# Performance work log

Measured on AMD Instinct MI355X. Metric: run time of the kernel, lower is better.

Reference implementation:

```python
import jax, jax.numpy as jnp
import numpy as np

B, N, D, H = 4, 4096, 1024, 16
DH = D // H            # 64
GH = 4 * DH            # gate hidden = 256
FREQ = N // 2 + 1      # 2049
INV_SQRT2 = 0.7071067811865476


def _ln(x, g, b, eps=1e-6):
    mu = jnp.mean(x, axis=-1, keepdims=True)
    var = jnp.mean((x - mu) ** 2, axis=-1, keepdims=True)
    return (x - mu) / jnp.sqrt(var + eps) * g + b


def _xavier(k, out_f, in_f, gain=0.8):
    bound = gain * (6.0 / (in_f + out_f)) ** 0.5
    return jax.random.uniform(k, (out_f, in_f), jnp.float32, -bound, bound)


def setup_inputs() -> dict:
    key = jax.random.key(0)
    ks = jax.random.split(key, 8)
    return {
        'x': jax.random.normal(ks[0], (B, N, D), jnp.float32),
        'Wq': _xavier(ks[1], D, D),
        'Wv': _xavier(ks[2], D, D),
        'Wo': _xavier(ks[3], D, D),
        'ln_g': jnp.ones((DH,), jnp.float32),
        'ln_b': jnp.zeros((DH,), jnp.float32),
        'Wgup': _xavier(ks[4], GH, DH),
        'Wgdn': _xavier(ks[5], 2 * FREQ, GH),
        'Wwup': _xavier(ks[6], GH, DH),
        'Wwdn': _xavier(ks[7], N, GH),
    }


def reference(x, Wq, Wv, Wo, ln_g, ln_b, Wgup, Wgdn, Wwup, Wwdn):
    Bx, Nx, Dx = x.shape
    # projections -> [B, H, N, DH]
    q = (x @ Wq.T).reshape(Bx, Nx, H, DH).transpose(0, 2, 1, 3)
    v = (x @ Wv.T).reshape(Bx, Nx, H, DH).transpose(0, 2, 1, 3)
    # per-head summary token -> complex spectral gate over FREQ bins
    bar = _ln(q.mean(axis=2), ln_g, ln_b)                    # [B, H, DH]
    gr = (jax.nn.silu(bar @ Wgup.T) @ Wgdn.T)               # [B, H, 2*FREQ]
    gr = gr.reshape(Bx, H, FREQ, 2)
    gate = jax.lax.complex(gr[..., 0], gr[..., 1])           # [B, H, FREQ]
    # spectral mixing (chunk == seq_len, power-of-two path)
    spec = jnp.fft.rfft(v, axis=2, norm='ortho') * gate[..., None]
    v_t = jnp.fft.irfft(spec, n=Nx, axis=2, norm='ortho')    # [B, H, N, DH]
    # Haar wavelet refinement
    even, odd = v_t[..., ::2, :], v_t[..., 1::2, :]
    w = jnp.concatenate([even + odd, even - odd], axis=-2) * INV_SQRT2
    s = (jax.nn.silu(bar @ Wwup.T) @ Wwdn.T)[..., None]      # [B, H, N, 1]
    w = w * s
    half = Nx // 2
    low, high = w[..., :half, :], w[..., half:, :]
    # interleave even/odd back along seq dim
    refine = jnp.stack([low + high, low - high], axis=-2).reshape(Bx, H, Nx, DH) * INV_SQRT2
    v_t = v_t + refine
    y = v_t.transpose(0, 2, 1, 3).reshape(Bx, Nx, Dx)
    return y @ Wo.T
```

## Files before the change

### kernel.cpp

```cpp
#include <hip/hip_runtime.h>

constexpr int CB = 4, CN = 4096, CD = 1024, CH = 16, CDH = 64, CGH = 256, CFREQ = 2049, CBH = 64;

constexpr size_t OFF_XSUM = 0;
constexpr size_t OFF_HG   = 4096;
constexpr size_t OFF_HW   = OFF_HG + (size_t)CBH * CGH;
constexpr size_t OFF_GATE = OFF_HW + (size_t)CBH * CGH;
constexpr size_t OFF_S    = OFF_GATE + (size_t)CBH * 2 * CFREQ;
constexpr size_t OFF_CA   = OFF_S + (size_t)CBH * CN;
constexpr size_t OFF_CD   = OFF_CA + (size_t)CBH * (CN / 2);
constexpr size_t OFF_TW   = OFF_CD + (size_t)CBH * (CN / 2);
constexpr size_t OFF_VCOL = OFF_TW + 8192;
constexpr size_t OFF_XHI  = OFF_VCOL + (size_t)CB * CD * CN;
constexpr size_t OFF_XLO  = OFF_XHI + (size_t)CB * CN * CD / 2;
constexpr size_t OFF_WVHI = OFF_XLO + (size_t)CB * CN * CD / 2;
constexpr size_t OFF_WVLO = OFF_WVHI + (size_t)CD * CD / 2;
constexpr size_t OFF_WOHI = OFF_WVLO + (size_t)CD * CD / 2;
constexpr size_t OFF_WOLO = OFF_WOHI + (size_t)CD * CD / 2;

typedef __bf16 bf16x8 __attribute__((ext_vector_type(8)));
typedef __bf16 bf16x4 __attribute__((ext_vector_type(4)));
typedef float  f32x4  __attribute__((ext_vector_type(4)));

__device__ __forceinline__ float silu_f(float x) { return x / (1.0f + expf(-x)); }

__device__ __forceinline__ void gload16(const void* g, void* l) {
    __builtin_amdgcn_global_load_lds(
        reinterpret_cast<const __attribute__((address_space(1))) unsigned int*>(
            reinterpret_cast<uintptr_t>(g)),
        reinterpret_cast<__attribute__((address_space(3))) unsigned int*>(
            reinterpret_cast<uintptr_t>(l)),
        16, 0, 0);
}

__device__ __forceinline__ float2 cadd(float2 a, float2 b) { return make_float2(a.x + b.x, a.y + b.y); }
__device__ __forceinline__ float2 csub(float2 a, float2 b) { return make_float2(a.x - b.x, a.y - b.y); }
__device__ __forceinline__ float2 cmul(float2 a, float2 b) { return make_float2(a.x * b.x - a.y * b.y, a.x * b.y + a.y * b.x); }
__device__ __forceinline__ float2 cmulc(float2 a, float2 b) { return make_float2(a.x * b.x + a.y * b.y, a.y * b.x - a.x * b.y); }
__device__ __forceinline__ float2 mulni(float2 a) { return make_float2(a.y, -a.x); }
__device__ __forceinline__ float2 mulpi(float2 a) { return make_float2(-a.y, a.x); }

__device__ __forceinline__ int fsw(int r) { return r ^ ((r >> 4) & 15); }

__device__ __forceinline__ int drev4(int k) {
    return ((k & 3) << 10) | (((k >> 2) & 3) << 8) | (((k >> 4) & 3) << 6)
         | (((k >> 6) & 3) << 4) | (((k >> 8) & 3) << 2) | ((k >> 10) & 3);
}

__global__ void k_tw(float* twf) {
    int i = blockIdx.x * 256 + threadIdx.x;
    if (i < 4096) {
        double ang = -2.0 * 3.14159265358979323846 * (double)i / 4096.0;
        twf[2 * i]     = (float)cos(ang);
        twf[2 * i + 1] = (float)sin(ang);
    }
}

__global__ __launch_bounds__(256) void k_meansplit(const float* __restrict__ X, float* __restrict__ xsum,
                                                   __bf16* __restrict__ hi, __bf16* __restrict__ lo) {
    int b = blockIdx.y;
    int c = blockIdx.x;
    int t = threadIdx.x;
    int half = t >> 7;
    int col = (t & 127) * 8;
    size_t base = (size_t)b * CN * CD + ((size_t)c * 64 + half * 32) * CD + col;
    float acc[8];
#pragma unroll
    for (int j = 0; j < 8; ++j) acc[j] = 0.f;
    for (int n = 0; n < 32; ++n) {
        size_t o = base + (size_t)n * CD;
        float4 v0 = *(const float4*)(X + o);
        float4 v1 = *(const float4*)(X + o + 4);
        float vv[8] = {v0.x, v0.y, v0.z, v0.w, v1.x, v1.y, v1.z, v1.w};
        bf16x8 hv, lv;
#pragma unroll
        for (int j = 0; j < 8; ++j) {
            acc[j] += vv[j];
            __bf16 h = (__bf16)vv[j];
            hv[j] = h;
            lv[j] = (__bf16)(vv[j] - (float)h);
        }
        *(bf16x8*)&hi[o] = hv;
        *(bf16x8*)&lo[o] = lv;
    }
#pragma unroll
    for (int j = 0; j < 8; ++j) atomicAdd(&xsum[b * CD + col + j], acc[j]);
}

__global__ __launch_bounds__(256) void k_barhidden(const float* __restrict__ xsum,
                                                   const float* __restrict__ Wq,
                                                   const float* __restrict__ ln_g,
                                                   const float* __restrict__ ln_b,
                                                   const float* __restrict__ Wgup,
                                                   const float* __restrict__ Wwup,
                                                   float* __restrict__ hg, float* __restrict__ hw) {
    int bh = blockIdx.x;
    int b = bh >> 4, h = bh & 15;
    int t = threadIdx.x;
    __shared__ float part[256];
    __shared__ float bar_s[64];
    int dh = t >> 2, seg = t & 3;
    const float* wrow = Wq + (size_t)(h * 64 + dh) * CD + seg * 256;
    const float* xs = xsum + b * CD + seg * 256;
    float acc = 0.f;
    for (int i = 0; i < 256; i += 4) {
        float4 w4 = *(const float4*)(wrow + i);
        float4 x4 = *(const float4*)(xs + i);
        acc += w4.x * x4.x + w4.y * x4.y + w4.z * x4.z + w4.w * x4.w;
    }
    part[t] = acc;
    __syncthreads();
    if (t < 64) {
        float q = (part[4 * t] + part[4 * t + 1] + part[4 * t + 2] + part[4 * t + 3]) * (1.0f / 4096.0f);
        float mu = q;
        for (int o = 32; o >= 1; o >>= 1) mu += __shfl_xor(mu, o, 64);
        mu *= (1.0f / 64.0f);
        float dev = q - mu;
        float vv = dev * dev;
        for (int o = 32; o >= 1; o >>= 1) vv += __shfl_xor(vv, o, 64);
        vv *= (1.0f / 64.0f);
        bar_s[t] = dev / sqrtf(vv + 1e-6f) * ln_g[t] + ln_b[t];
    }
    __syncthreads();
    const float* gup = Wgup + (size_t)t * CDH;
    const float* wup = Wwup + (size_t)t * CDH;
    float ag = 0.f, aw = 0.f;
    for (int i = 0; i < CDH; i += 4) {
        float4 bb = *(const float4*)(&bar_s[i]);
        float4 g4 = *(const float4*)(gup + i);
        float4 w4 = *(const float4*)(wup + i);
        ag += g4.x * bb.x + g4.y * bb.y + g4.z * bb.z + g4.w * bb.w;
        aw += w4.x * bb.x + w4.y * bb.y + w4.z * bb.z + w4.w * bb.w;
    }
    hg[bh * CGH + t] = silu_f(ag);
    hw[bh * CGH + t] = silu_f(aw);
}

__global__ __launch_bounds__(256) void k_gategemv(const float* __restrict__ Wgdn,
                                                  const float* __restrict__ Wwdn,
                                                  const float* __restrict__ hg,
                                                  const float* __restrict__ hw,
                                                  float* __restrict__ gate, float* __restrict__ sbuf) {
    int z = blockIdx.z;
    const float* Wd = z ? Wwdn : Wgdn;
    const float* hid = z ? hw : hg;
    float* out = z ? sbuf : gate;
    int Kout = z ? CN : 2 * CFREQ;
    int bh0 = blockIdx.y * 8;
    int t = threadIdx.x;
    int k = blockIdx.x * 256 + t;
    __shared__ float Lh[8][256];
    for (int g = 0; g < 8; ++g) Lh[g][t] = hid[(size_t)(bh0 + g) * CGH + t];
    __syncthreads();
    if (k >= Kout) return;
    float accv[8] = {0.f, 0.f, 0.f, 0.f, 0.f, 0.f, 0.f, 0.f};
    const float* wrow = Wd + (size_t)k * CGH;
    for (int j4 = 0; j4 < 64; ++j4) {
        float4 wv = *(const float4*)(wrow + 4 * j4);
#pragma unroll
        for (int g = 0; g < 8; ++g) {
            accv[g] += wv.x * Lh[g][4 * j4] + wv.y * Lh[g][4 * j4 + 1] +
                       wv.z * Lh[g][4 * j4 + 2] + wv.w * Lh[g][4 * j4 + 3];
        }
    }
    for (int g = 0; g < 8; ++g) out[(size_t)(bh0 + g) * Kout + k] = accv[g];
}

__global__ __launch_bounds__(256) void k_coef(const float* __restrict__ sbuf,
                                              float* __restrict__ ca, float* __restrict__ cd) {
    int bh = blockIdx.y;
    int i = blockIdx.x * 256 + threadIdx.x;
    float s0 = sbuf[(size_t)bh * CN + i];
    float s1 = sbuf[(size_t)bh * CN + 2048 + i];
    ca[(size_t)bh * 2048 + i] = 1.0f + 0.5f * (s0 + s1);
    cd[(size_t)bh * 2048 + i] = 0.5f * (s0 - s1);
}

__global__ __launch_bounds__(256) void k_split(const float* __restrict__ src,
                                               __bf16* __restrict__ hi, __bf16* __restrict__ lo,
                                               int n4) {
    int i = blockIdx.x * 256 + threadIdx.x;
    int stride = gridDim.x * 256;
    for (; i < n4; i += stride) {
        float4 v = ((const float4*)src)[i];
        __bf16 h0 = (__bf16)v.x, h1 = (__bf16)v.y, h2 = (__bf16)v.z, h3 = (__bf16)v.w;
        bf16x4 hv = {h0, h1, h2, h3};
        bf16x4 lv = {(__bf16)(v.x - (float)h0), (__bf16)(v.y - (float)h1),
                     (__bf16)(v.z - (float)h2), (__bf16)(v.w - (float)h3)};
        *(bf16x4*)&hi[4 * (size_t)i] = hv;
        *(bf16x4*)&lo[4 * (size_t)i] = lv;
    }
}

__global__ __launch_bounds__(256) void k_tsplit(const float* __restrict__ Vcol,
                                                __bf16* __restrict__ hi, __bf16* __restrict__ lo) {
    __shared__ float tile[32][33];
    int bx = blockIdx.x;
    int by = blockIdx.y;
    int b  = blockIdx.z;
    int t = threadIdx.x;
    int d = t >> 3, n4 = (t & 7) * 4;
    const float* src = Vcol + ((size_t)b * CD + by * 32 + d) * CN + bx * 32 + n4;
    float4 v = *(const float4*)src;
    tile[d][n4] = v.x; tile[d][n4 + 1] = v.y; tile[d][n4 + 2] = v.z; tile[d][n4 + 3] = v.w;
    __syncthreads();
    int n = t >> 3, d4 = (t & 7) * 4;
    size_t o = ((size_t)b * CN + bx * 32 + n) * CD + by * 32 + d4;
    float x0 = tile[d4][n], x1 = tile[d4 + 1][n], x2 = tile[d4 + 2][n], x3 = tile[d4 + 3][n];
    __bf16 h0 = (__bf16)x0, h1 = (__bf16)x1, h2 = (__bf16)x2, h3 = (__bf16)x3;
    bf16x4 hv = {h0, h1, h2, h3};
    bf16x4 lv = {(__bf16)(x0 - (float)h0), (__bf16)(x1 - (float)h1),
                 (__bf16)(x2 - (float)h2), (__bf16)(x3 - (float)h3)};
    *(bf16x4*)&hi[o] = hv;
    *(bf16x4*)&lo[o] = lv;
}

template <int TRANS>
__global__ __launch_bounds__(256) void k_mfma_gemm(const __bf16* __restrict__ Ahi,
                                                   const __bf16* __restrict__ Alo,
                                                   const __bf16* __restrict__ Bhi,
                                                   const __bf16* __restrict__ Blo,
                                                   float* __restrict__ C) {
    __shared__ __align__(16) __bf16 lds[2][4][128 * 32];
    int t = threadIdx.x;
    int l = t & 63, w = t >> 6;
    int hw = blockIdx.x + (blockIdx.y << 3);
    int xcd = hw & 7, slot = hw >> 3;
    int m0 = (xcd * 16 + (slot >> 3)) * 128;
    int n0 = (slot & 7) * 128;
    int wm = w >> 1, wn = w & 1;

    const __bf16* gsrc = (w == 0) ? Ahi : (w == 1) ? Alo : (w == 2) ? Bhi : Blo;
    int gr0 = (w < 2) ? m0 : n0;
    unsigned o[8];
#pragma unroll
    for (int i = 0; i < 8; ++i) {
        int row = i * 16 + (l >> 2);
        unsigned slotq = (unsigned)((l & 3) ^ ((row >> 2) & 3));
        o[i] = (unsigned)(gr0 + row) * 1024u + slotq * 8u;
    }

    f32x4 acc[4][4];
#pragma unroll
    for (int m = 0; m < 4; ++m)
#pragma unroll
        for (int n = 0; n < 4; ++n) acc[m][n] = (f32x4){0.f, 0.f, 0.f, 0.f};

#pragma unroll
    for (int i = 0; i < 8; ++i)
        gload16(gsrc + (size_t)o[i], &lds[0][w][i * 512]);
    __syncthreads();

    int cur = 0;
#pragma unroll 2
    for (int k0 = 0; k0 < 1024; k0 += 32) {
        if (k0 + 32 < 1024) {
#pragma unroll
            for (int i = 0; i < 8; ++i)
                gload16(gsrc + ((size_t)o[i] + k0 + 32), &lds[cur ^ 1][w][i * 512]);
        }

        bf16x8 ah[4], al[4], bh[4], bl[4];
#pragma unroll
        for (int m = 0; m < 4; ++m) {
            int row = wm * 64 + m * 16 + (l & 15);
            int sl = (l >> 4) ^ ((row >> 2) & 3);
            ah[m] = *(const bf16x8*)&lds[cur][0][row * 32 + sl * 8];
            al[m] = *(const bf16x8*)&lds[cur][1][row * 32 + sl * 8];
        }
#pragma unroll
        for (int n = 0; n < 4; ++n) {
            int row = wn * 64 + n * 16 + (l & 15);
            int sl = (l >> 4) ^ ((row >> 2) & 3);
            bh[n] = *(const bf16x8*)&lds[cur][2][row * 32 + sl * 8];
            bl[n] = *(const bf16x8*)&lds[cur][3][row * 32 + sl * 8];
        }
#pragma unroll
        for (int m = 0; m < 4; ++m)
#pragma unroll
            for (int n = 0; n < 4; ++n) {
                acc[m][n] = __builtin_amdgcn_mfma_f32_16x16x32_bf16(ah[m], bh[n], acc[m][n], 0, 0, 0);
                acc[m][n] = __builtin_amdgcn_mfma_f32_16x16x32_bf16(ah[m], bl[n], acc[m][n], 0, 0, 0);
                acc[m][n] = __builtin_amdgcn_mfma_f32_16x16x32_bf16(al[m], bh[n], acc[m][n], 0, 0, 0);
            }
        __syncthreads();
        cur ^= 1;
    }

    if (TRANS) {
        int b = m0 >> 12;
        int tokb = (m0 & 4095) + wm * 64;
#pragma unroll
        for (int m = 0; m < 4; ++m)
#pragma unroll
            for (int n = 0; n < 4; ++n) {
                int dcol = n0 + wn * 64 + n * 16 + (l & 15);
                int tok = tokb + m * 16 + ((l >> 4) << 2);
                *(f32x4*)&C[((size_t)(b * CD + dcol)) * CN + tok] = acc[m][n];
            }
    } else {
#pragma unroll
        for (int m = 0; m < 4; ++m)
#pragma unroll
            for (int n = 0; n < 4; ++n) {
                int r0 = m0 + wm * 64 + m * 16 + ((l >> 4) << 2);
                int cc = n0 + wn * 64 + n * 16 + (l & 15);
#pragma unroll
                for (int q = 0; q < 4; ++q) C[(size_t)(r0 + q) * CD + cc] = acc[m][n][q];
            }
    }
}

__global__ __launch_bounds__(512) void k_fft(float* __restrict__ Vcol,
                                             const float* __restrict__ gateB,
                                             const float* __restrict__ caB,
                                             const float* __restrict__ cdB,
                                             const float2* __restrict__ tw) {
    __shared__ float2 buf[4096];
    int blk = blockIdx.x;
    int bh = blk >> 5, pr = blk & 31;
    int t = threadIdx.x;
    float* colA = Vcol + (size_t)(bh * 64 + pr * 2) * CN;
    float* colB = colA + CN;

    for (int n = t; n < 4096; n += 512) buf[fsw(n)] = make_float2(colA[n], colB[n]);
    __syncthreads();

#pragma unroll 1
    for (int M = 1024; M >= 1; M >>= 2) {
        int tstep = 1024 / M;
        for (int idx = t; idx < 1024; idx += 512) {
            int j = idx & (M - 1);
            int i0 = ((idx & ~(M - 1)) << 2) + j;
            float2 a0 = buf[fsw(i0)];
            float2 a1 = buf[fsw(i0 + M)];
            float2 a2 = buf[fsw(i0 + 2 * M)];
            float2 a3 = buf[fsw(i0 + 3 * M)];
            float2 t0 = cadd(a0, a2), t1 = csub(a0, a2);
            float2 t2 = cadd(a1, a3), t3 = csub(a1, a3);
            float2 w1 = tw[j * tstep], w2 = tw[2 * j * tstep], w3 = tw[3 * j * tstep];
            buf[fsw(i0)]         = cadd(t0, t2);
            buf[fsw(i0 + M)]     = cmul(cadd(t1, mulni(t3)), w1);
            buf[fsw(i0 + 2 * M)] = cmul(csub(t0, t2), w2);
            buf[fsw(i0 + 3 * M)] = cmul(cadd(t1, mulpi(t3)), w3);
        }
        __syncthreads();
    }

    const float2* g2 = (const float2*)gateB + (size_t)bh * CFREQ;
    for (int k = t; k <= 2048; k += 512) {
        int r  = drev4(k);
        int r2 = drev4((4096 - k) & 4095);
        float2 Zk = buf[fsw(r)];
        float2 Zj = buf[fsw(r2)];
        float2 Av = make_float2(0.5f * (Zk.x + Zj.x), 0.5f * (Zk.y - Zj.y));
        float2 Bv = make_float2(0.5f * (Zk.y + Zj.y), -0.5f * (Zk.x - Zj.x));
        float2 g = g2[k];
        float2 SA = cmul(g, Av);
        float2 SB = cmul(g, Bv);
        buf[fsw(r)] = make_float2(SA.x - SB.y, SA.y + SB.x);
        if (r2 != r) buf[fsw(r2)] = make_float2(SA.x + SB.y, SB.x - SA.y);
    }
    __syncthreads();

#pragma unroll 1
    for (int M = 1; M <= 1024; M <<= 2) {
        int tstep = 1024 / M;
        for (int idx = t; idx < 1024; idx += 512) {
            int j = idx & (M - 1);
            int i0 = ((idx & ~(M - 1)) << 2) + j;
            float2 a0 = buf[fsw(i0)];
            float2 a1 = cmulc(buf[fsw(i0 + M)], tw[j * tstep]);
            float2 a2 = cmulc(buf[fsw(i0 + 2 * M)], tw[2 * j * tstep]);
            float2 a3 = cmulc(buf[fsw(i0 + 3 * M)], tw[3 * j * tstep]);
            float2 t0 = cadd(a0, a2), t1 = csub(a0, a2);
            float2 t2 = cadd(a1, a3), t3 = csub(a1, a3);
            buf[fsw(i0)]         = cadd(t0, t2);
            buf[fsw(i0 + M)]     = cadd(t1, mulpi(t3));
            buf[fsw(i0 + 2 * M)] = csub(t0, t2);
            buf[fsw(i0 + 3 * M)] = csub(t1, mulpi(t3));
        }
        __syncthreads();
    }

    const float scale = 1.0f / 4096.0f;
    const float* ca = caB + (size_t)bh * 2048;
    const float* cd = cdB + (size_t)bh * 2048;
    for (int i = t; i < 2048; i += 512) {
        float2 v0 = buf[fsw(2 * i)], v1 = buf[fsw(2 * i + 1)];
        float a0x = v0.x * scale, a1x = v1.x * scale;
        float a0y = v0.y * scale, a1y = v1.y * scale;
        float A_ = ca[i], D_ = cd[i];
        *(float2*)(colA + 2 * i) = make_float2(A_ * a0x + D_ * a1x, D_ * a0x + A_ * a1x);
        *(float2*)(colB + 2 * i) = make_float2(A_ * a0y + D_ * a1y, D_ * a0y + A_ * a1y);
    }
}

extern "C" void kernel_launch(void* const* d_in, const int* in_sizes, int n_in,
                              void* d_out, int out_size, void* d_ws, size_t ws_size,
                              hipStream_t stream) {
    const float* x    = (const float*)d_in[0];
    const float* Wq   = (const float*)d_in[1];
    const float* Wv   = (const float*)d_in[2];
    const float* Wo   = (const float*)d_in[3];
    const float* ln_g = (const float*)d_in[4];
    const float* ln_b = (const float*)d_in[5];
    const float* Wgup = (const float*)d_in[6];
    const float* Wgdn = (const float*)d_in[7];
    const float* Wwup = (const float*)d_in[8];
    const float* Wwdn = (const float*)d_in[9];
    float* ws  = (float*)d_ws;
    float* out = (float*)d_out;

    __bf16* xhi  = (__bf16*)(ws + OFF_XHI);
    __bf16* xlo  = (__bf16*)(ws + OFF_XLO);
    __bf16* wvhi = (__bf16*)(ws + OFF_WVHI);
    __bf16* wvlo = (__bf16*)(ws + OFF_WVLO);
    __bf16* wohi = (__bf16*)(ws + OFF_WOHI);
    __bf16* wolo = (__bf16*)(ws + OFF_WOLO);
    __bf16* v2hi = (__bf16*)(ws + OFF_XHI);
    __bf16* v2lo = (__bf16*)(ws + OFF_XLO);

    hipMemsetAsync(ws + OFF_XSUM, 0, 4096 * sizeof(float), stream);
    k_tw<<<16, 256, 0, stream>>>(ws + OFF_TW);
    k_meansplit<<<dim3(64, 4), 256, 0, stream>>>(x, ws + OFF_XSUM, xhi, xlo);
    k_barhidden<<<64, 256, 0, stream>>>(ws + OFF_XSUM, Wq, ln_g, ln_b, Wgup, Wwup,
                                        ws + OFF_HG, ws + OFF_HW);
    k_gategemv<<<dim3(17, 8, 2), 256, 0, stream>>>(Wgdn, Wwdn, ws + OFF_HG, ws + OFF_HW,
                                                   ws + OFF_GATE, ws + OFF_S);
    k_coef<<<dim3(8, 64), 256, 0, stream>>>(ws + OFF_S, ws + OFF_CA, ws + OFF_CD);

    k_split<<<1024, 256, 0, stream>>>(Wv, wvhi, wvlo, CD * CD / 4);
    k_split<<<1024, 256, 0, stream>>>(Wo, wohi, wolo, CD * CD / 4);

    k_mfma_gemm<1><<<dim3(8, 128), 256, 0, stream>>>(xhi, xlo, wvhi, wvlo, ws + OFF_VCOL);

    k_fft<<<2048, 512, 0, stream>>>(ws + OFF_VCOL, ws + OFF_GATE, ws + OFF_CA, ws + OFF_CD,
                                    (const float2*)(ws + OFF_TW));

    k_tsplit<<<dim3(128, 32, 4), 256, 0, stream>>>(ws + OFF_VCOL, v2hi, v2lo);

    k_mfma_gemm<0><<<dim3(8, 128), 256, 0, stream>>>(v2hi, v2lo, wohi, wolo, out);
}
```

Measured before the change: 425.6 us.

## Switch spectral FFT from radix-4 to radix-8 with fused first and last stages

Replaces the six-stage radix-4 shared-memory FFT with a four-stage radix-8 decomposition. The first forward stage runs straight from global loads and the last inverse stage feeds the Haar refinement output through lane shuffles, so fewer LDS round trips and barriers are needed. LDS indexing changes from an XOR swizzle to a padded layout, and the scale factor is folded into the wavelet coefficients. This raises register pressure per thread and depends on the twiddle table indexing and the radix-8 digit-reversal being correct.

```diff
diff --git a/kernel.cpp b/kernel.cpp
--- a/kernel.cpp
+++ b/kernel.cpp
@@ -40,11 +40,78 @@
 __device__ __forceinline__ float2 mulni(float2 a) { return make_float2(a.y, -a.x); }
 __device__ __forceinline__ float2 mulpi(float2 a) { return make_float2(-a.y, a.x); }
 
-__device__ __forceinline__ int fsw(int r) { return r ^ ((r >> 4) & 15); }
-
-__device__ __forceinline__ int drev4(int k) {
-    return ((k & 3) << 10) | (((k >> 2) & 3) << 8) | (((k >> 4) & 3) << 6)
-         | (((k >> 6) & 3) << 4) | (((k >> 8) & 3) << 2) | ((k >> 10) & 3);
+__device__ __forceinline__ int P(int r) { return r + (r >> 3); }
+
+__device__ __forceinline__ int drev8(int k) {
+    return ((k & 7) << 9) | (((k >> 3) & 7) << 6) | (((k >> 6) & 7) << 3) | ((k >> 9) & 7);
+}
+
+__device__ __forceinline__ void dft8_fwd(const float2 a[8], float2 A[8]) {
+    float2 t0 = cadd(a[0], a[4]), t1 = csub(a[0], a[4]);
+    float2 t2 = cadd(a[2], a[6]), t3 = mulni(csub(a[2], a[6]));
+    float2 t4 = cadd(a[1], a[5]), t5 = csub(a[1], a[5]);
+    float2 t6 = cadd(a[3], a[7]), t7 = mulni(csub(a[3], a[7]));
+    float2 u0 = cadd(t0, t2), u1 = csub(t0, t2);
+    float2 u2 = cadd(t1, t3), u3 = csub(t1, t3);
+    float2 u4 = cadd(t4, t6), u5 = mulni(csub(t4, t6));
+    float2 u6 = cadd(t5, t7), u7 = csub(t5, t7);
+    const float s = 0.70710678118654752f;
+    float2 w6 = make_float2(s * (u6.x + u6.y), s * (u6.y - u6.x));
+    float2 w7 = make_float2(s * (u7.y - u7.x), -s * (u7.x + u7.y));
+    A[0] = cadd(u0, u4); A[4] = csub(u0, u4);
+    A[2] = cadd(u1, u5); A[6] = csub(u1, u5);
+    A[1] = cadd(u2, w6); A[5] = csub(u2, w6);
+    A[3] = cadd(u3, w7); A[7] = csub(u3, w7);
+}
+
+__device__ __forceinline__ void dft8_inv(const float2 a[8], float2 A[8]) {
+    float2 t0 = cadd(a[0], a[4]), t1 = csub(a[0], a[4]);
+    float2 t2 = cadd(a[2], a[6]), t3 = mulpi(csub(a[2], a[6]));
+    float2 t4 = cadd(a[1], a[5]), t5 = csub(a[1], a[5]);
+    float2 t6 = cadd(a[3], a[7]), t7 = mulpi(csub(a[3], a[7]));
+    float2 u0 = cadd(t0, t2), u1 = csub(t0, t2);
+    float2 u2 = cadd(t1, t3), u3 = csub(t1, t3);
+    float2 u4 = cadd(t4, t6), u5 = mulpi(csub(t4, t6));
+    float2 u6 = cadd(t5, t7), u7 = csub(t5, t7);
+    const float s = 0.70710678118654752f;
+    float2 w6 = make_float2(s * (u6.x - u6.y), s * (u6.x + u6.y));
+    float2 w7 = make_float2(-s * (u7.x + u7.y), s * (u7.x - u7.y));
+    A[0] = cadd(u0, u4); A[4] = csub(u0, u4);
+    A[2] = cadd(u1, u5); A[6] = csub(u1, u5);
+    A[1] = cadd(u2, w6); A[5] = csub(u2, w6);
+    A[3] = cadd(u3, w7); A[7] = csub(u3, w7);
+}
+
+template <int M>
+__device__ __forceinline__ void fwd_stage(float2* buf, const float2* __restrict__ tw, int t) {
+    int j = t & (M - 1);
+    int i0 = ((t & ~(M - 1)) << 3) + j;
+    constexpr int TS = 512 / M;
+    float2 a[8], A[8];
+#pragma unroll
+    for (int c = 0; c < 8; ++c) a[c] = buf[P(i0 + c * M)];
+    dft8_fwd(a, A);
+#pragma unroll
+    for (int p = 0; p < 8; ++p) {
+        float2 v = (M > 1 && p) ? cmul(A[p], tw[j * p * TS]) : A[p];
+        buf[P(i0 + p * M)] = v;
+    }
+}
+
+template <int M>
+__device__ __forceinline__ void inv_stage(float2* buf, const float2* __restrict__ tw, int t) {
+    int j = t & (M - 1);
+    int i0 = ((t & ~(M - 1)) << 3) + j;
+    constexpr int TS = 512 / M;
+    float2 a[8], A[8];
+#pragma unroll
+    for (int c = 0; c < 8; ++c) {
+        float2 v = buf[P(i0 + c * M)];
+        a[c] = (M > 1 && c) ? cmulc(v, tw[j * c * TS]) : v;
+    }
+    dft8_inv(a, A);
+#pragma unroll
+    for (int p = 0; p < 8; ++p) buf[P(i0 + p * M)] = A[p];
 }
 
 __global__ void k_tw(float* twf) {
@@ -316,83 +383,75 @@
                                              const float* __restrict__ caB,
                                              const float* __restrict__ cdB,
                                              const float2* __restrict__ tw) {
-    __shared__ float2 buf[4096];
+    __shared__ float2 buf[4608];
     int blk = blockIdx.x;
     int bh = blk >> 5, pr = blk & 31;
     int t = threadIdx.x;
     float* colA = Vcol + (size_t)(bh * 64 + pr * 2) * CN;
     float* colB = colA + CN;
 
-    for (int n = t; n < 4096; n += 512) buf[fsw(n)] = make_float2(colA[n], colB[n]);
-    __syncthreads();
-
-#pragma unroll 1
-    for (int M = 1024; M >= 1; M >>= 2) {
-        int tstep = 1024 / M;
-        for (int idx = t; idx < 1024; idx += 512) {
-            int j = idx & (M - 1);
-            int i0 = ((idx & ~(M - 1)) << 2) + j;
-            float2 a0 = buf[fsw(i0)];
-            float2 a1 = buf[fsw(i0 + M)];
-            float2 a2 = buf[fsw(i0 + 2 * M)];
-            float2 a3 = buf[fsw(i0 + 3 * M)];
-            float2 t0 = cadd(a0, a2), t1 = csub(a0, a2);
-            float2 t2 = cadd(a1, a3), t3 = csub(a1, a3);
-            float2 w1 = tw[j * tstep], w2 = tw[2 * j * tstep], w3 = tw[3 * j * tstep];
-            buf[fsw(i0)]         = cadd(t0, t2);
-            buf[fsw(i0 + M)]     = cmul(cadd(t1, mulni(t3)), w1);
-            buf[fsw(i0 + 2 * M)] = cmul(csub(t0, t2), w2);
-            buf[fsw(i0 + 3 * M)] = cmul(cadd(t1, mulpi(t3)), w3);
-        }
-        __syncthreads();
-    }
-
-    const float2* g2 = (const float2*)gateB + (size_t)bh * CFREQ;
-    for (int k = t; k <= 2048; k += 512) {
-        int r  = drev4(k);
-        int r2 = drev4((4096 - k) & 4095);
-        float2 Zk = buf[fsw(r)];
-        float2 Zj = buf[fsw(r2)];
-        float2 Av = make_float2(0.5f * (Zk.x + Zj.x), 0.5f * (Zk.y - Zj.y));
-        float2 Bv = make_float2(0.5f * (Zk.y + Zj.y), -0.5f * (Zk.x - Zj.x));
-        float2 g = g2[k];
-        float2 SA = cmul(g, Av);
-        float2 SB = cmul(g, Bv);
-        buf[fsw(r)] = make_float2(SA.x - SB.y, SA.y + SB.x);
-        if (r2 != r) buf[fsw(r2)] = make_float2(SA.x + SB.y, SB.x - SA.y);
-    }
-    __syncthreads();
-
-#pragma unroll 1
-    for (int M = 1; M <= 1024; M <<= 2) {
-        int tstep = 1024 / M;
-        for (int idx = t; idx < 1024; idx += 512) {
-            int j = idx & (M - 1);
-            int i0 = ((idx & ~(M - 1)) << 2) + j;
-            float2 a0 = buf[fsw(i0)];
-            float2 a1 = cmulc(buf[fsw(i0 + M)], tw[j * tstep]);
-            float2 a2 = cmulc(buf[fsw(i0 + 2 * M)], tw[2 * j * tstep]);
-            float2 a3 = cmulc(buf[fsw(i0 + 3 * M)], tw[3 * j * tstep]);
-            float2 t0 = cadd(a0, a2), t1 = csub(a0, a2);
-            float2 t2 = cadd(a1, a3), t3 = csub(a1, a3);
-            buf[fsw(i0)]         = cadd(t0, t2);
-            buf[fsw(i0 + M)]     = cadd(t1, mulpi(t3));
-            buf[fsw(i0 + 2 * M)] = csub(t0, t2);
-            buf[fsw(i0 + 3 * M)] = csub(t1, mulpi(t3));
-        }
-        __syncthreads();
-    }
-
-    const float scale = 1.0f / 4096.0f;
-    const float* ca = caB + (size_t)bh * 2048;
-    const float* cd = cdB + (size_t)bh * 2048;
-    for (int i = t; i < 2048; i += 512) {
-        float2 v0 = buf[fsw(2 * i)], v1 = buf[fsw(2 * i + 1)];
-        float a0x = v0.x * scale, a1x = v1.x * scale;
-        float a0y = v0.y * scale, a1y = v1.y * scale;
-        float A_ = ca[i], D_ = cd[i];
-        *(float2*)(colA + 2 * i) = make_float2(A_ * a0x + D_ * a1x, D_ * a0x + A_ * a1x);
-        *(float2*)(colB + 2 * i) = make_float2(A_ * a0y + D_ * a1y, D_ * a0y + A_ * a1y);
+    {
+        float2 a[8], A[8];
+#pragma unroll
+        for (int c = 0; c < 8; ++c) {
+            int n = t + 512 * c;
+            a[c] = make_float2(colA[n], colB[n]);
+        }
+        dft8_fwd(a, A);
+#pragma unroll
+        for (int p = 0; p < 8; ++p) {
+            float2 v = p ? cmul(A[p], tw[t * p]) : A[p];
+            buf[P(t + 512 * p)] = v;
+        }
+    }
+    __syncthreads();
+    fwd_stage<64>(buf, tw, t);  __syncthreads();
+    fwd_stage<8>(buf, tw, t);   __syncthreads();
+    fwd_stage<1>(buf, tw, t);   __syncthreads();
+
+    {
+        const float2* g2 = (const float2*)gateB + (size_t)bh * CFREQ;
+        for (int k = t; k <= 2048; k += 512) {
+            int r  = drev8(k);
+            int r2 = drev8((4096 - k) & 4095);
+            float2 Zk = buf[P(r)];
+            float2 Zj = buf[P(r2)];
+            float2 Av = make_float2(0.5f * (Zk.x + Zj.x), 0.5f * (Zk.y - Zj.y));
+            float2 Bv = make_float2(0.5f * (Zk.y + Zj.y), -0.5f * (Zk.x - Zj.x));
+            float2 g = g2[k];
+            float2 SA = cmul(g, Av);
+            float2 SB = cmul(g, Bv);
+            buf[P(r)] = make_float2(SA.x - SB.y, SA.y + SB.x);
+            if (r2 != r) buf[P(r2)] = make_float2(SA.x + SB.y, SB.x - SA.y);
+        }
+    }
+    __syncthreads();
+
+    inv_stage<1>(buf, tw, t);   __syncthreads();
+    inv_stage<8>(buf, tw, t);   __syncthreads();
+    inv_stage<64>(buf, tw, t);  __syncthreads();
+
+    {
+        float2 a[8], A[8];
+#pragma unroll
+        for (int c = 0; c < 8; ++c) {
+            float2 v = buf[P(t + 512 * c)];
+            a[c] = c ? cmulc(v, tw[t * c]) : v;
+        }
+        dft8_inv(a, A);
+        const float scale = 1.0f / 4096.0f;
+        const float* ca = caB + (size_t)bh * 2048;
+        const float* cd = cdB + (size_t)bh * 2048;
+#pragma unroll
+        for (int p = 0; p < 8; ++p) {
+            int n = t + 512 * p;
+            int i = n >> 1;
+            float A_ = ca[i] * scale, D_ = cd[i] * scale;
+            float ox = __shfl_xor(A[p].x, 1, 64);
+            float oy = __shfl_xor(A[p].y, 1, 64);
+            colA[n] = A_ * A[p].x + D_ * ox;
+            colB[n] = A_ * A[p].y + D_ * oy;
+        }
     }
 }
 
```

Result: faster. 416.7 us (-2.1%).
